# Optimization experiments

Measured on AMD Instinct MI355X. Metric: run time of the kernel, lower is better.

Reference implementation:

```python
import jax, jax.numpy as jnp
import numpy as np

B, N, E = 128, 2000, 2000
EMBED, HIDDEN = 256, 512


def setup_inputs() -> dict:
    key = jax.random.key(0)
    k1, k2, k3, k4, k5, k6, k7 = jax.random.split(key, 7)
    node_embeddings = jax.random.normal(k1, (B, N, EMBED), dtype=jnp.float32)
    locs = jax.random.uniform(k2, (B, N, 2), dtype=jnp.float32)
    edge_list = jax.random.randint(k3, (B, E, 2), 0, N, dtype=jnp.int64)
    in_dim = 2 * EMBED + 1
    # Kaiming-ish init for the two Linear layers of edge_scorer
    W1 = jax.random.normal(k4, (in_dim, HIDDEN), dtype=jnp.float32) / np.sqrt(in_dim)
    b1 = jnp.zeros((HIDDEN,), dtype=jnp.float32)
    W2 = jax.random.normal(k5, (HIDDEN, 1), dtype=jnp.float32) / np.sqrt(HIDDEN)
    b2 = jnp.zeros((1,), dtype=jnp.float32)
    return {
        "node_embeddings": node_embeddings,
        "locs": locs,
        "edge_list": edge_list,
        "delete_bias": 0,
        "W1": W1,
        "b1": b1,
        "W2": W2,
        "b2": b2,
    }


def reference(node_embeddings, locs, edge_list, delete_bias, W1, b1, W2, b2):
    # valid mask for -1-padded edges
    valid = (edge_list[..., 0] >= 0) & (edge_list[..., 1] >= 0)  # (B, E)
    edges = jnp.clip(edge_list, 0, None)
    bidx = jnp.arange(node_embeddings.shape[0])[:, None]  # (B, 1)
    i, j = edges[..., 0], edges[..., 1]  # (B, E)
    emb_i = node_embeddings[bidx, i]  # (B, E, D)
    emb_j = node_embeddings[bidx, j]  # (B, E, D)
    d = locs[bidx, i] - locs[bidx, j]  # (B, E, 2)
    dist = jnp.sqrt(jnp.sum(d * d, axis=-1, keepdims=True))  # (B, E, 1)
    feats = jnp.concatenate([emb_i, emb_j, dist], axis=-1)  # (B, E, 2D+1)
    h = jax.nn.relu(jnp.einsum('bef,fh->beh', feats, W1) + b1)
    logits = (jnp.einsum('beh,ho->beo', h, W2) + b2)[..., 0]  # (B, E)
    logits = jnp.where(valid, logits, -jnp.inf)
    return logits + jnp.float32(delete_bias)
```

## Files before the change

kernel.cpp:

```cpp
#include <hip/hip_runtime.h>
#include <math.h>

#define EMBED    256
#define HIDDEN   512
#define Nn       2000
#define Ee       2000
#define BM       128
#define TILES    8
#define NBLK     250
#define NTHREADS 512
#define FP       264

typedef __attribute__((ext_vector_type(8)))  short bf16x8;
typedef __attribute__((ext_vector_type(16))) float f32x16;

static __device__ __forceinline__ short f2bf(float f) {
  unsigned u = __builtin_bit_cast(unsigned, f);
  u += 0x7fffu + ((u >> 16) & 1u);
  return (short)(u >> 16);
}

static __device__ __forceinline__ bf16x8 cvt8(float4 a, float4 b) {
  bf16x8 v;
  v[0]=f2bf(a.x); v[1]=f2bf(a.y); v[2]=f2bf(a.z); v[3]=f2bf(a.w);
  v[4]=f2bf(b.x); v[5]=f2bf(b.y); v[6]=f2bf(b.z); v[7]=f2bf(b.w);
  return v;
}

#define LBAR() do { asm volatile("s_waitcnt lgkmcnt(0)" ::: "memory"); \
                    __builtin_amdgcn_s_barrier(); \
                    asm volatile("" ::: "memory"); } while (0)

__global__ void w1f_kernel(const float* __restrict__ W1, short* __restrict__ W1F) {
  const int t  = blockIdx.x * 512 + threadIdx.x;
  const int l  = t & 63;
  const int tk = (t >> 6) & 31;
  const int tn = t >> 11;
  const int n  = tn * 32 + (l & 31);
  const int k0 = tk * 16 + (l >> 5) * 8;
  bf16x8 v;
#pragma unroll
  for (int q = 0; q < 8; ++q)
    v[q] = f2bf(W1[(size_t)(k0 + q) * HIDDEN + n]);
  *(bf16x8*)(W1F + (size_t)t * 8) = v;
}

__global__ __launch_bounds__(NTHREADS, 2)
void edge_kernel(const float* __restrict__ emb, const float* __restrict__ locs,
                 const int* __restrict__ edges, const int* __restrict__ dbias,
                 const float* __restrict__ W1, const float* __restrict__ b1,
                 const float* __restrict__ W2, const float* __restrict__ b2,
                 const short* __restrict__ W1F, float* __restrict__ out)
{
  __shared__ short feat[2][BM][FP];
  __shared__ float b1_s[HIDDEN], w513_s[HIDDEN], w2_s[HIDDEN];
  __shared__ float part_s[8][64];
  __shared__ float dist_s[2][BM];
  __shared__ int   valid_s[2][BM];
  __shared__ int   ibase_s[2][BM], jbase_s[2][BM];

  const int tid = threadIdx.x;

  const int orig = blockIdx.x;
  const int xcd  = orig & 7;
  const int idx  = orig >> 3;
  const int sbid = (xcd < 2 ? xcd * 32 : 64 + (xcd - 2) * 31) + idx;
  const int eblk = sbid * (TILES * BM);

  b1_s[tid]   = b1[tid];
  w513_s[tid] = W1[(size_t)512 * HIDDEN + tid];
  w2_s[tid]   = W2[tid];
  const float b2s_base = b2[0] + (float)dbias[0];

  auto do_meta = [&](int T) {
    const int g  = eblk + T * BM + tid;
    const int b  = g / Ee;
    const int i0 = edges[2 * g];
    const int j0 = edges[2 * g + 1];
    valid_s[T & 1][tid] = (i0 >= 0) && (j0 >= 0);
    const int ib = b * Nn + (i0 < 0 ? 0 : i0);
    const int jb = b * Nn + (j0 < 0 ? 0 : j0);
    ibase_s[T & 1][tid] = ib;
    jbase_s[T & 1][tid] = jb;
    const float dx = locs[2 * (size_t)ib]     - locs[2 * (size_t)jb];
    const float dy = locs[2 * (size_t)ib + 1] - locs[2 * (size_t)jb + 1];
    dist_s[T & 1][tid] = sqrtf(dx * dx + dy * dy);
  };

  if (tid < BM) do_meta(0);
  LBAR();

  const int sq = tid & 7;
  const int ehs = tid >> 3;
  const int lane = tid & 63;
  const int w    = tid >> 6;
  const int eh   = w & 1;
  const int ng   = w >> 1;
  const int ln31 = lane & 31;
  const int kg   = lane >> 5;

#pragma unroll
  for (int r = 0; r < 2; ++r) {
    const int el = r * 64 + ehs;
    const float* src = emb + (size_t)ibase_s[0][el] * EMBED + sq * 8;
#pragma unroll
    for (int m = 0; m < 4; ++m) {
      float4 a  = *(const float4*)(src + m * 64);
      float4 b4 = *(const float4*)(src + m * 64 + 4);
      *(bf16x8*)&feat[0][el][(sq + 8 * m) * 8] = cvt8(a, b4);
    }
  }
  LBAR();

  f32x16 acc[2][4];
#pragma unroll
  for (int et = 0; et < 2; ++et)
#pragma unroll
    for (int nt = 0; nt < 4; ++nt)
#pragma unroll
      for (int q = 0; q < 16; ++q) acc[et][nt][q] = 0.f;

  const short* wfb = W1F + (size_t)(ng * 4 * 32) * 512 + lane * 8;

#pragma unroll 1
  for (int p = 0; p < 2 * TILES; ++p) {
    const int bb   = p & 1;
    const int nbuf = bb ^ 1;
    const int half = p & 1;
    const int tps  = (p + 1) >> 1;
    const int sh   = (p + 1) & 1;
    const bool stg = p < 2 * TILES - 1;

    bf16x8 wc[4], wn[4];
#pragma unroll
    for (int nt = 0; nt < 4; ++nt)
      wc[nt] = *(const bf16x8*)(wfb + (size_t)(nt * 32 + half * 16) * 512);

    float4 hg00, hg01, hg10, hg11;

#pragma unroll
    for (int ks = 0; ks < 16; ++ks) {
      if (ks < 15) {
#pragma unroll
        for (int nt = 0; nt < 4; ++nt)
          wn[nt] = *(const bf16x8*)(wfb + (size_t)(nt * 32 + half * 16 + ks + 1) * 512);
      }

      if (stg && (ks & 3) == 0) {
        const int g2 = ks >> 2;
        const int el = (g2 >> 1) * 64 + ehs;
        const int rb = sh ? jbase_s[tps & 1][el] : ibase_s[tps & 1][el];
        const float* src = emb + (size_t)rb * EMBED + sq * 8 + (g2 & 1) * 128;
        hg00 = *(const float4*)(src);
        hg01 = *(const float4*)(src + 4);
        hg10 = *(const float4*)(src + 64);
        hg11 = *(const float4*)(src + 68);
      }
      if (stg && (ks & 3) == 3) {
        const int g2 = ks >> 2;
        const int el = (g2 >> 1) * 64 + ehs;
        const int mb = (g2 & 1) * 2;
        *(bf16x8*)&feat[nbuf][el][(sq + 8 * mb) * 8]       = cvt8(hg00, hg01);
        *(bf16x8*)&feat[nbuf][el][(sq + 8 * (mb + 1)) * 8] = cvt8(hg10, hg11);
      }
      if ((p & 1) == 0 && ks == 1 && tid < BM && (p >> 1) + 1 < TILES)
        do_meta((p >> 1) + 1);

      bf16x8 fb0 = *(const bf16x8*)(&feat[bb][eh * 64 + ln31][ks * 16 + kg * 8]);
      bf16x8 fb1 = *(const bf16x8*)(&feat[bb][eh * 64 + 32 + ln31][ks * 16 + kg * 8]);

      __builtin_amdgcn_s_setprio(1);
#pragma unroll
      for (int nt = 0; nt < 4; ++nt) {
        acc[0][nt] = __builtin_amdgcn_mfma_f32_32x32x16_bf16(wc[nt], fb0, acc[0][nt], 0, 0, 0);
        acc[1][nt] = __builtin_amdgcn_mfma_f32_32x32x16_bf16(wc[nt], fb1, acc[1][nt], 0, 0, 0);
      }
      __builtin_amdgcn_s_setprio(0);
#pragma unroll
      for (int nt = 0; nt < 4; ++nt) wc[nt] = wn[nt];
    }
    LBAR();

    if (p & 1) {
      const int t   = p >> 1;
      const int mb2 = t & 1;
      float dv[2], ps[2];
#pragma unroll
      for (int et = 0; et < 2; ++et) {
        dv[et] = dist_s[mb2][eh * 64 + et * 32 + ln31];
        ps[et] = 0.f;
      }
#pragma unroll
      for (int nt = 0; nt < 4; ++nt) {
#pragma unroll
        for (int r = 0; r < 16; ++r) {
          const int n = ng * 128 + nt * 32 + (r & 3) + ((r >> 2) << 3) + (kg << 2);
          const float bias = b1_s[n];
          const float wd   = w513_s[n];
          const float w2v  = w2_s[n];
#pragma unroll
          for (int et = 0; et < 2; ++et) {
            float pv = acc[et][nt][r] + bias + dv[et] * wd;
            ps[et] += fmaxf(pv, 0.f) * w2v;
          }
        }
      }
#pragma unroll
      for (int et = 0; et < 2; ++et) ps[et] += __shfl_xor(ps[et], 32, 64);
      if (lane < 32) {
#pragma unroll
        for (int et = 0; et < 2; ++et) part_s[w][et * 32 + ln31] = ps[et];
      }
      LBAR();
      if (tid < BM) {
        const int ehh = tid >> 6;
        const int es  = tid & 63;
        float s = part_s[ehh][es] + part_s[2 + ehh][es] +
                  part_s[4 + ehh][es] + part_s[6 + ehh][es];
        float logit = s + b2s_base;
        if (!valid_s[mb2][tid]) logit = -__builtin_inff();
        out[eblk + t * BM + tid] = logit;
      }
#pragma unroll
      for (int et = 0; et < 2; ++et)
#pragma unroll
        for (int nt = 0; nt < 4; ++nt)
#pragma unroll
          for (int q = 0; q < 16; ++q) acc[et][nt][q] = 0.f;
    }
  }
}

extern "C" void kernel_launch(void* const* d_in, const int* in_sizes, int n_in,
                              void* d_out, int out_size, void* d_ws, size_t ws_size,
                              hipStream_t stream) {
  const float* emb   = (const float*)d_in[0];
  const float* locs  = (const float*)d_in[1];
  const int*   edges = (const int*)d_in[2];
  const int*   dbias = (const int*)d_in[3];
  const float* W1    = (const float*)d_in[4];
  const float* b1    = (const float*)d_in[5];
  const float* W2    = (const float*)d_in[6];
  const float* b2    = (const float*)d_in[7];
  float*       out   = (float*)d_out;
  short*       W1F   = (short*)d_ws;

  w1f_kernel<<<dim3(64), dim3(512), 0, stream>>>(W1, W1F);
  edge_kernel<<<dim3(NBLK), dim3(NTHREADS), 0, stream>>>(
      emb, locs, edges, dbias, W1, b1, W2, b2, (const short*)W1F, out);
}
```

Baseline: 162.8 us.

## Warp-specialize edge kernel into MFMA consumer and gather producer waves

Splits the 8 waves into 4 compute waves, each covering 128 hidden units over 64-edge tiles, and 4 producer waves that gather and convert embeddings, compute metadata, and write outputs. A triple-buffered LDS ring of 64-edge by 64-k chunks lets producers stay two chunks ahead of the MFMA waves. The goal is to take global gather latency and bf16 conversion off the compute waves' critical path. In exchange only half the waves issue MFMAs, there is a block barrier per small chunk, and each W1 fragment now feeds half as many edges, so L2 weight traffic per edge doubles.

```diff
diff --git a/kernel.cpp b/kernel.cpp
--- a/kernel.cpp
+++ b/kernel.cpp
@@ -5,11 +5,12 @@
 #define HIDDEN   512
 #define Nn       2000
 #define Ee       2000
-#define BM       128
-#define TILES    8
+#define BMT      64
+#define TILES    16
 #define NBLK     250
 #define NTHREADS 512
-#define FP       264
+#define NCHUNK   (TILES * 8)
+#define FP       72
 
 typedef __attribute__((ext_vector_type(8)))  short bf16x8;
 typedef __attribute__((ext_vector_type(16))) float f32x16;
@@ -52,12 +53,12 @@
                  const float* __restrict__ W2, const float* __restrict__ b2,
                  const short* __restrict__ W1F, float* __restrict__ out)
 {
-  __shared__ short feat[2][BM][FP];
+  __shared__ short feat[3][BMT][FP];
   __shared__ float b1_s[HIDDEN], w513_s[HIDDEN], w2_s[HIDDEN];
-  __shared__ float part_s[8][64];
-  __shared__ float dist_s[2][BM];
-  __shared__ int   valid_s[2][BM];
-  __shared__ int   ibase_s[2][BM], jbase_s[2][BM];
+  __shared__ float part_s[2][4][BMT];
+  __shared__ float dist_s[2][BMT];
+  __shared__ int   valid_s[2][BMT];
+  __shared__ int   ibase_s[2][BMT], jbase_s[2][BMT];
 
   const int tid = threadIdx.x;
 
@@ -65,51 +66,55 @@
   const int xcd  = orig & 7;
   const int idx  = orig >> 3;
   const int sbid = (xcd < 2 ? xcd * 32 : 64 + (xcd - 2) * 31) + idx;
-  const int eblk = sbid * (TILES * BM);
+  const int eblk = sbid * (TILES * BMT);
 
   b1_s[tid]   = b1[tid];
   w513_s[tid] = W1[(size_t)512 * HIDDEN + tid];
   w2_s[tid]   = W2[tid];
   const float b2s_base = b2[0] + (float)dbias[0];
 
+  const int lane = tid & 63;
+  const int w    = tid >> 6;
+  const int ln31 = lane & 31;
+  const int kg   = lane >> 5;
+
+  const int pt = tid - 256;
+  const int e  = pt >> 2;
+  const int sq = pt & 3;
+
   auto do_meta = [&](int T) {
-    const int g  = eblk + T * BM + tid;
+    const int g  = eblk + T * BMT + pt;
     const int b  = g / Ee;
     const int i0 = edges[2 * g];
     const int j0 = edges[2 * g + 1];
-    valid_s[T & 1][tid] = (i0 >= 0) && (j0 >= 0);
+    valid_s[T & 1][pt] = (i0 >= 0) && (j0 >= 0);
     const int ib = b * Nn + (i0 < 0 ? 0 : i0);
     const int jb = b * Nn + (j0 < 0 ? 0 : j0);
-    ibase_s[T & 1][tid] = ib;
-    jbase_s[T & 1][tid] = jb;
+    ibase_s[T & 1][pt] = ib;
+    jbase_s[T & 1][pt] = jb;
     const float dx = locs[2 * (size_t)ib]     - locs[2 * (size_t)jb];
     const float dy = locs[2 * (size_t)ib + 1] - locs[2 * (size_t)jb + 1];
-    dist_s[T & 1][tid] = sqrtf(dx * dx + dy * dy);
+    dist_s[T & 1][pt] = sqrtf(dx * dx + dy * dy);
   };
 
-  if (tid < BM) do_meta(0);
+  auto stage = [&](int gc, int buf) {
+    const int T    = gc >> 3;
+    const int ph   = gc & 7;
+    const int side = ph >> 2;
+    const int q    = ph & 3;
+    const int rb = side ? jbase_s[T & 1][e] : ibase_s[T & 1][e];
+    const float* src = emb + (size_t)rb * EMBED + q * 64 + sq * 16;
+    float4 g0 = *(const float4*)(src);
+    float4 g1 = *(const float4*)(src + 4);
+    float4 g2 = *(const float4*)(src + 8);
+    float4 g3 = *(const float4*)(src + 12);
+    *(bf16x8*)&feat[buf][e][sq * 16]     = cvt8(g0, g1);
+    *(bf16x8*)&feat[buf][e][sq * 16 + 8] = cvt8(g2, g3);
+  };
+
+  if (w >= 4 && pt < BMT) do_meta(0);
   LBAR();
-
-  const int sq = tid & 7;
-  const int ehs = tid >> 3;
-  const int lane = tid & 63;
-  const int w    = tid >> 6;
-  const int eh   = w & 1;
-  const int ng   = w >> 1;
-  const int ln31 = lane & 31;
-  const int kg   = lane >> 5;
-
-#pragma unroll
-  for (int r = 0; r < 2; ++r) {
-    const int el = r * 64 + ehs;
-    const float* src = emb + (size_t)ibase_s[0][el] * EMBED + sq * 8;
-#pragma unroll
-    for (int m = 0; m < 4; ++m) {
-      float4 a  = *(const float4*)(src + m * 64);
-      float4 b4 = *(const float4*)(src + m * 64 + 4);
-      *(bf16x8*)&feat[0][el][(sq + 8 * m) * 8] = cvt8(a, b4);
-    }
-  }
+  if (w >= 4) { stage(0, 0); stage(1, 1); }
   LBAR();
 
   f32x16 acc[2][4];
@@ -120,114 +125,98 @@
 #pragma unroll
       for (int q = 0; q < 16; ++q) acc[et][nt][q] = 0.f;
 
-  const short* wfb = W1F + (size_t)(ng * 4 * 32) * 512 + lane * 8;
+  const short* wfb = W1F + (size_t)(w * 4 * 32) * 512 + lane * 8;
 
 #pragma unroll 1
-  for (int p = 0; p < 2 * TILES; ++p) {
-    const int bb   = p & 1;
-    const int nbuf = bb ^ 1;
-    const int half = p & 1;
-    const int tps  = (p + 1) >> 1;
-    const int sh   = (p + 1) & 1;
-    const bool stg = p < 2 * TILES - 1;
-
-    bf16x8 wc[4], wn[4];
-#pragma unroll
-    for (int nt = 0; nt < 4; ++nt)
-      wc[nt] = *(const bf16x8*)(wfb + (size_t)(nt * 32 + half * 16) * 512);
-
-    float4 hg00, hg01, hg10, hg11;
-
-#pragma unroll
-    for (int ks = 0; ks < 16; ++ks) {
-      if (ks < 15) {
-#pragma unroll
-        for (int nt = 0; nt < 4; ++nt)
-          wn[nt] = *(const bf16x8*)(wfb + (size_t)(nt * 32 + half * 16 + ks + 1) * 512);
-      }
-
-      if (stg && (ks & 3) == 0) {
-        const int g2 = ks >> 2;
-        const int el = (g2 >> 1) * 64 + ehs;
-        const int rb = sh ? jbase_s[tps & 1][el] : ibase_s[tps & 1][el];
-        const float* src = emb + (size_t)rb * EMBED + sq * 8 + (g2 & 1) * 128;
-        hg00 = *(const float4*)(src);
-        hg01 = *(const float4*)(src + 4);
-        hg10 = *(const float4*)(src + 64);
-        hg11 = *(const float4*)(src + 68);
-      }
-      if (stg && (ks & 3) == 3) {
-        const int g2 = ks >> 2;
-        const int el = (g2 >> 1) * 64 + ehs;
-        const int mb = (g2 & 1) * 2;
-        *(bf16x8*)&feat[nbuf][el][(sq + 8 * mb) * 8]       = cvt8(hg00, hg01);
-        *(bf16x8*)&feat[nbuf][el][(sq + 8 * (mb + 1)) * 8] = cvt8(hg10, hg11);
-      }
-      if ((p & 1) == 0 && ks == 1 && tid < BM && (p >> 1) + 1 < TILES)
-        do_meta((p >> 1) + 1);
-
-      bf16x8 fb0 = *(const bf16x8*)(&feat[bb][eh * 64 + ln31][ks * 16 + kg * 8]);
-      bf16x8 fb1 = *(const bf16x8*)(&feat[bb][eh * 64 + 32 + ln31][ks * 16 + kg * 8]);
-
-      __builtin_amdgcn_s_setprio(1);
-#pragma unroll
-      for (int nt = 0; nt < 4; ++nt) {
-        acc[0][nt] = __builtin_amdgcn_mfma_f32_32x32x16_bf16(wc[nt], fb0, acc[0][nt], 0, 0, 0);
-        acc[1][nt] = __builtin_amdgcn_mfma_f32_32x32x16_bf16(wc[nt], fb1, acc[1][nt], 0, 0, 0);
-      }
-      __builtin_amdgcn_s_setprio(0);
-#pragma unroll
-      for (int nt = 0; nt < 4; ++nt) wc[nt] = wn[nt];
+  for (int p = 0; p < NCHUNK; ++p) {
+    const int buf = p % 3;
+
+    if (w < 4) {
+      const int tk0 = (p & 7) * 4;
+      bf16x8 wc[4], wn[4];
+#pragma unroll
+      for (int nt = 0; nt < 4; ++nt)
+        wc[nt] = *(const bf16x8*)(wfb + (size_t)(nt * 32 + tk0) * 512);
+#pragma unroll
+      for (int ks = 0; ks < 4; ++ks) {
+        if (ks < 3) {
+#pragma unroll
+          for (int nt = 0; nt < 4; ++nt)
+            wn[nt] = *(const bf16x8*)(wfb + (size_t)(nt * 32 + tk0 + ks + 1) * 512);
+        }
+        bf16x8 fb0 = *(const bf16x8*)(&feat[buf][ln31][ks * 16 + kg * 8]);
+        bf16x8 fb1 = *(const bf16x8*)(&feat[buf][32 + ln31][ks * 16 + kg * 8]);
+        __builtin_amdgcn_s_setprio(1);
+#pragma unroll
+        for (int nt = 0; nt < 4; ++nt) {
+          acc[0][nt] = __builtin_amdgcn_mfma_f32_32x32x16_bf16(wc[nt], fb0, acc[0][nt], 0, 0, 0);
+          acc[1][nt] = __builtin_amdgcn_mfma_f32_32x32x16_bf16(wc[nt], fb1, acc[1][nt], 0, 0, 0);
+        }
+        __builtin_amdgcn_s_setprio(0);
+#pragma unroll
+        for (int nt = 0; nt < 4; ++nt) wc[nt] = wn[nt];
+      }
+
+      if ((p & 7) == 7) {
+        const int T   = p >> 3;
+        const int par = T & 1;
+        float dv[2], ps[2];
+#pragma unroll
+        for (int et = 0; et < 2; ++et) {
+          dv[et] = dist_s[par][et * 32 + ln31];
+          ps[et] = 0.f;
+        }
+#pragma unroll
+        for (int nt = 0; nt < 4; ++nt) {
+#pragma unroll
+          for (int r = 0; r < 16; ++r) {
+            const int n = w * 128 + nt * 32 + (r & 3) + ((r >> 2) << 3) + (kg << 2);
+            const float bias = b1_s[n];
+            const float wd   = w513_s[n];
+            const float w2v  = w2_s[n];
+#pragma unroll
+            for (int et = 0; et < 2; ++et) {
+              float pv = acc[et][nt][r] + bias + dv[et] * wd;
+              ps[et] += fmaxf(pv, 0.f) * w2v;
+            }
+          }
+        }
+#pragma unroll
+        for (int et = 0; et < 2; ++et) ps[et] += __shfl_xor(ps[et], 32, 64);
+        if (lane < 32) {
+#pragma unroll
+          for (int et = 0; et < 2; ++et) part_s[par][w][et * 32 + ln31] = ps[et];
+        }
+#pragma unroll
+        for (int et = 0; et < 2; ++et)
+#pragma unroll
+          for (int nt = 0; nt < 4; ++nt)
+#pragma unroll
+            for (int q = 0; q < 16; ++q) acc[et][nt][q] = 0.f;
+      }
+    } else {
+      if (((p + 3) & 7) == 0) {
+        const int T = (p + 3) >> 3;
+        if (T < TILES && pt < BMT) do_meta(T);
+      }
+      if (p + 2 < NCHUNK) stage(p + 2, (p + 2) % 3);
+      if ((p & 7) == 0 && p > 0 && pt < BMT) {
+        const int S   = (p >> 3) - 1;
+        const int par = S & 1;
+        float s = part_s[par][0][pt] + part_s[par][1][pt] +
+                  part_s[par][2][pt] + part_s[par][3][pt] + b2s_base;
+        if (!valid_s[par][pt]) s = -__builtin_inff();
+        out[eblk + S * BMT + pt] = s;
+      }
     }
     LBAR();
-
-    if (p & 1) {
-      const int t   = p >> 1;
-      const int mb2 = t & 1;
-      float dv[2], ps[2];
-#pragma unroll
-      for (int et = 0; et < 2; ++et) {
-        dv[et] = dist_s[mb2][eh * 64 + et * 32 + ln31];
-        ps[et] = 0.f;
-      }
-#pragma unroll
-      for (int nt = 0; nt < 4; ++nt) {
-#pragma unroll
-        for (int r = 0; r < 16; ++r) {
-          const int n = ng * 128 + nt * 32 + (r & 3) + ((r >> 2) << 3) + (kg << 2);
-          const float bias = b1_s[n];
-          const float wd   = w513_s[n];
-          const float w2v  = w2_s[n];
-#pragma unroll
-          for (int et = 0; et < 2; ++et) {
-            float pv = acc[et][nt][r] + bias + dv[et] * wd;
-            ps[et] += fmaxf(pv, 0.f) * w2v;
-          }
-        }
-      }
-#pragma unroll
-      for (int et = 0; et < 2; ++et) ps[et] += __shfl_xor(ps[et], 32, 64);
-      if (lane < 32) {
-#pragma unroll
-        for (int et = 0; et < 2; ++et) part_s[w][et * 32 + ln31] = ps[et];
-      }
-      LBAR();
-      if (tid < BM) {
-        const int ehh = tid >> 6;
-        const int es  = tid & 63;
-        float s = part_s[ehh][es] + part_s[2 + ehh][es] +
-                  part_s[4 + ehh][es] + part_s[6 + ehh][es];
-        float logit = s + b2s_base;
-        if (!valid_s[mb2][tid]) logit = -__builtin_inff();
-        out[eblk + t * BM + tid] = logit;
-      }
-#pragma unroll
-      for (int et = 0; et < 2; ++et)
-#pragma unroll
-        for (int nt = 0; nt < 4; ++nt)
-#pragma unroll
-          for (int q = 0; q < 16; ++q) acc[et][nt][q] = 0.f;
-    }
+  }
+
+  if (w >= 4 && pt < BMT) {
+    float s = part_s[1][0][pt] + part_s[1][1][pt] +
+              part_s[1][2][pt] + part_s[1][3][pt] + b2s_base;
+    if (!valid_s[1][pt]) s = -__builtin_inff();
+    out[eblk + (TILES - 1) * BMT + pt] = s;
   }
 }
 
```

Result: slower. 209.4 us (+28.6%).
